# Kernel optimization log

Measured on AMD Instinct MI355X. Metric: run time of the kernel, lower is better.

Reference implementation:

```python
import jax, jax.numpy as jnp
import numpy as np

N_NODES = 100000
N_EDGES = 1600000
D_FEAT = 256
D_HID = 256


def setup_inputs() -> dict:
    key = jax.random.key(0)
    ks = jax.random.split(key, 8)
    x = jax.random.normal(ks[0], (N_NODES, D_FEAT), dtype=jnp.float32)
    src = jax.random.randint(ks[1], (N_EDGES,), 0, N_NODES, dtype=jnp.int32)
    dst = jax.random.randint(ks[2], (N_EDGES,), 0, N_NODES, dtype=jnp.int32)
    s = 1.0 / np.sqrt(D_FEAT)
    W_self1 = jax.random.normal(ks[3], (D_FEAT, D_HID), dtype=jnp.float32) * s
    W_neigh1 = jax.random.normal(ks[4], (D_FEAT, D_HID), dtype=jnp.float32) * s
    b1 = jnp.zeros((D_HID,), dtype=jnp.float32)
    s2 = 1.0 / np.sqrt(D_HID)
    W_self2 = jax.random.normal(ks[5], (D_HID, 1), dtype=jnp.float32) * s2
    W_neigh2 = jax.random.normal(ks[6], (D_HID, 1), dtype=jnp.float32) * s2
    b2 = jnp.zeros((1,), dtype=jnp.float32)
    return {"x": x, "src": src, "dst": dst,
            "W_self1": W_self1, "W_neigh1": W_neigh1, "b1": b1,
            "W_self2": W_self2, "W_neigh2": W_neigh2, "b2": b2}


def _mean_aggregate(h, src, dst, n_nodes):
    # sum of neighbor features per destination node, then divide by in-degree (clamped to 1)
    msg = jax.ops.segment_sum(h[src], dst, num_segments=n_nodes)  # [N, d]
    deg = jax.ops.segment_sum(jnp.ones((src.shape[0],), dtype=h.dtype), dst,
                              num_segments=n_nodes)
    return msg / jnp.maximum(deg, 1.0)[:, None]


def _sage_layer(h, src, dst, W_self, W_neigh, b):
    # DGL SAGEConv('mean'): h_dst @ W_self + mean_neigh(h_src) @ W_neigh + b
    neigh = _mean_aggregate(h, src, dst, h.shape[0])
    return h @ W_self + neigh @ W_neigh + b


def reference(x, src, dst, W_self1, W_neigh1, b1, W_self2, W_neigh2, b2):
    h = _sage_layer(x, src, dst, W_self1, W_neigh1, b1)
    h = jax.nn.sigmoid(h)  # F.sigmoid activation; dropout is identity in eval
    h = _sage_layer(h, src, dst, W_self2, W_neigh2, b2)  # [N, 1]
    return h
```

## Files before the change

### kernel.cpp

```cpp
#include <hip/hip_runtime.h>
#include <hip/hip_bf16.h>

typedef __attribute__((ext_vector_type(8))) short short8;
typedef __attribute__((ext_vector_type(4))) float f32x4;

__device__ __forceinline__ unsigned short f2b(float f) {
    union { float f; unsigned int u; } v; v.f = f;
    unsigned int u = v.u;
    unsigned int r = (u + 0x7fffu + ((u >> 16) & 1u)) >> 16;
    return (unsigned short)r;
}
__device__ __forceinline__ float b2f(unsigned int h) {
    union { unsigned int u; float f; } v; v.u = h << 16; return v.f;
}
__device__ __forceinline__ void acc8(uint4 v, float* a) {
    a[0] += b2f(v.x & 0xffffu); a[1] += b2f(v.x >> 16);
    a[2] += b2f(v.y & 0xffffu); a[3] += b2f(v.y >> 16);
    a[4] += b2f(v.z & 0xffffu); a[5] += b2f(v.z >> 16);
    a[6] += b2f(v.w & 0xffffu); a[7] += b2f(v.w >> 16);
}

#define DF 256
#define KK2 512
#define EPT 8
#define BCAP 8192

__global__ void k_convx(const float* __restrict__ x, unsigned short* __restrict__ xb, int total) {
    int i = (blockIdx.x * blockDim.x + threadIdx.x) * 8;
    if (i >= total) return;
    float4 v0 = *(const float4*)(x + i);
    float4 v1 = *(const float4*)(x + i + 4);
    uint4 o;
    o.x = (unsigned)f2b(v0.x) | ((unsigned)f2b(v0.y) << 16);
    o.y = (unsigned)f2b(v0.z) | ((unsigned)f2b(v0.w) << 16);
    o.z = (unsigned)f2b(v1.x) | ((unsigned)f2b(v1.y) << 16);
    o.w = (unsigned)f2b(v1.z) | ((unsigned)f2b(v1.w) << 16);
    *(uint4*)(xb + i) = o;
}

__global__ void k_buildw(const float* __restrict__ Ws1, const float* __restrict__ Wn1,
                         unsigned short* __restrict__ Wt) {
    int tid = blockIdx.x * blockDim.x + threadIdx.x;
    int n = tid >> 9, k = tid & 511;
    float v = (k < DF) ? Ws1[k * DF + n] : Wn1[(k - DF) * DF + n];
    Wt[tid] = f2b(v);
}

__global__ void k_ginit(int* __restrict__ gcur, int NB) {
    int t = blockIdx.x * blockDim.x + threadIdx.x;
    if (t < NB) gcur[t * 16] = 0;
}

__global__ __launch_bounds__(256) void k_bin(const int* __restrict__ src, const int* __restrict__ dst,
                                             int* __restrict__ gcur, unsigned* __restrict__ colidx2, int E) {
    __shared__ int cnt[512];
    int t = threadIdx.x;
    int base = blockIdx.x * (256 * EPT);
    for (int b = t; b < 512; b += 256) cnt[b] = 0;
    __syncthreads();
    unsigned pk[EPT];
#pragma unroll
    for (int i = 0; i < EPT; ++i) {
        int idx = base + t + i * 256;
        unsigned w = 0xffffffffu;
        if (idx < E) {
            int d = dst[idx];
            int b = d >> 8, dl = d & 255;
            int r = atomicAdd(&cnt[b], 1);
            w = ((unsigned)dl << 22) | ((unsigned)b << 13) | (unsigned)r;
        }
        pk[i] = w;
    }
    __syncthreads();
    for (int b = t; b < 512; b += 256) {
        int c = cnt[b];
        if (c > 0) cnt[b] = atomicAdd(&gcur[b * 16], c);
    }
    __syncthreads();
#pragma unroll
    for (int i = 0; i < EPT; ++i) {
        unsigned w = pk[i];
        if (w == 0xffffffffu) continue;
        int idx = base + t + i * 256;
        int b = (w >> 13) & 0x1FF;
        int pos = cnt[b] + (int)(w & 0x1FFF);
        if (pos < BCAP)
            colidx2[(size_t)b * BCAP + pos] = ((w >> 22) << 17) | (unsigned)src[idx];
    }
}

__global__ __launch_bounds__(512) void k_bscan(const int* __restrict__ gcur, int* __restrict__ bbase,
                                               int* __restrict__ rowptr, int NB, int N) {
    __shared__ int sm[512];
    int t = threadIdx.x;
    int c = (t < NB) ? gcur[t * 16] : 0;
    if (c > BCAP) c = BCAP;
    sm[t] = c; __syncthreads();
    for (int off = 1; off < 512; off <<= 1) {
        int u = (t >= off) ? sm[t - off] : 0;
        __syncthreads();
        sm[t] += u;
        __syncthreads();
    }
    if (t < NB) bbase[t] = sm[t] - c;
    if (t == NB - 1) rowptr[N] = sm[t];
}

__global__ __launch_bounds__(256) void k_bsort(const unsigned* __restrict__ colidx2,
                                               const int* __restrict__ gcur,
                                               const int* __restrict__ bbase,
                                               int* __restrict__ rowptr,
                                               int* __restrict__ colidx, int N) {
    __shared__ unsigned ent[BCAP];
    __shared__ unsigned short rnk[BCAP];
    __shared__ int cnt2[256], sc[256];
    int b = blockIdx.x, t = threadIdx.x;
    int lo = b << 8;
    int n = gcur[b * 16]; if (n > BCAP) n = BCAP;
    int start = bbase[b];
    const unsigned* reg = colidx2 + (size_t)b * BCAP;
    for (int i = t; i < n; i += 256) ent[i] = reg[i];
    cnt2[t] = 0;
    __syncthreads();
    for (int i = t; i < n; i += 256) {
        int d = ent[i] >> 17;
        rnk[i] = (unsigned short)atomicAdd(&cnt2[d], 1);
    }
    __syncthreads();
    int v = cnt2[t]; sc[t] = v; __syncthreads();
    for (int off = 1; off < 256; off <<= 1) {
        int u = (t >= off) ? sc[t - off] : 0;
        __syncthreads();
        sc[t] += u;
        __syncthreads();
    }
    int exc = sc[t] - v;
    if (lo + t < N) rowptr[lo + t] = start + exc;
    __syncthreads();
    sc[t] = exc;
    __syncthreads();
    for (int i = t; i < n; i += 256) {
        unsigned w = ent[i];
        int d = w >> 17;
        colidx[start + sc[d] + rnk[i]] = (int)(w & 0x1FFFFu);
    }
}

__global__ void k_agg(const unsigned short* __restrict__ xb, const int* __restrict__ rowptr,
                      const int* __restrict__ colidx, unsigned short* __restrict__ nb, int N) {
    int w = (blockIdx.x * blockDim.x + threadIdx.x) >> 6;
    int lane = threadIdx.x & 63;
    if (w >= N) return;
    int s = rowptr[w], e = rowptr[w + 1];
    int half = lane >> 5, l2 = lane & 31;
    const unsigned short* base = xb + l2 * 8;
    float a[8] = {0.f, 0.f, 0.f, 0.f, 0.f, 0.f, 0.f, 0.f};
    int j = s;
    for (; j + 15 < e; j += 16) {
        int c0 = colidx[j + half];
        int c1 = colidx[j + 2 + half];
        int c2 = colidx[j + 4 + half];
        int c3 = colidx[j + 6 + half];
        int c4 = colidx[j + 8 + half];
        int c5 = colidx[j + 10 + half];
        int c6 = colidx[j + 12 + half];
        int c7 = colidx[j + 14 + half];
        uint4 v0 = *(const uint4*)(base + (size_t)c0 * DF);
        uint4 v1 = *(const uint4*)(base + (size_t)c1 * DF);
        uint4 v2 = *(const uint4*)(base + (size_t)c2 * DF);
        uint4 v3 = *(const uint4*)(base + (size_t)c3 * DF);
        uint4 v4 = *(const uint4*)(base + (size_t)c4 * DF);
        uint4 v5 = *(const uint4*)(base + (size_t)c5 * DF);
        uint4 v6 = *(const uint4*)(base + (size_t)c6 * DF);
        uint4 v7 = *(const uint4*)(base + (size_t)c7 * DF);
        acc8(v0, a); acc8(v1, a); acc8(v2, a); acc8(v3, a);
        acc8(v4, a); acc8(v5, a); acc8(v6, a); acc8(v7, a);
    }
    for (; j + 7 < e; j += 8) {
        int c0 = colidx[j + half];
        int c1 = colidx[j + 2 + half];
        int c2 = colidx[j + 4 + half];
        int c3 = colidx[j + 6 + half];
        uint4 v0 = *(const uint4*)(base + (size_t)c0 * DF);
        uint4 v1 = *(const uint4*)(base + (size_t)c1 * DF);
        uint4 v2 = *(const uint4*)(base + (size_t)c2 * DF);
        uint4 v3 = *(const uint4*)(base + (size_t)c3 * DF);
        acc8(v0, a); acc8(v1, a); acc8(v2, a); acc8(v3, a);
    }
    for (; j + 3 < e; j += 4) {
        int c0 = colidx[j + half];
        int c1 = colidx[j + 2 + half];
        uint4 v0 = *(const uint4*)(base + (size_t)c0 * DF);
        uint4 v1 = *(const uint4*)(base + (size_t)c1 * DF);
        acc8(v0, a); acc8(v1, a);
    }
    for (; j + 1 < e; j += 2) {
        int c = colidx[j + half];
        uint4 v = *(const uint4*)(base + (size_t)c * DF);
        acc8(v, a);
    }
    if (j < e && half == 0) {
        int c = colidx[j];
        uint4 v = *(const uint4*)(base + (size_t)c * DF);
        acc8(v, a);
    }
#pragma unroll
    for (int i = 0; i < 8; ++i) a[i] += __shfl_xor(a[i], 32);
    if (half == 0) {
        float r = 1.0f / (float)((e - s) > 1 ? (e - s) : 1);
        uint4 o;
        o.x = (unsigned)f2b(a[0] * r) | ((unsigned)f2b(a[1] * r) << 16);
        o.y = (unsigned)f2b(a[2] * r) | ((unsigned)f2b(a[3] * r) << 16);
        o.z = (unsigned)f2b(a[4] * r) | ((unsigned)f2b(a[5] * r) << 16);
        o.w = (unsigned)f2b(a[6] * r) | ((unsigned)f2b(a[7] * r) << 16);
        *(uint4*)(nb + (size_t)w * DF + l2 * 8) = o;
    }
}

__global__ __launch_bounds__(512) void k_gemm(const unsigned short* __restrict__ xb,
                                              const unsigned short* __restrict__ nbm,
                                              const unsigned short* __restrict__ Wt,
                                              const float* __restrict__ b1,
                                              const float* __restrict__ Ws2,
                                              const float* __restrict__ Wn2,
                                              float* __restrict__ sv,
                                              float* __restrict__ tv, int M) {
    __shared__ __align__(16) unsigned short As[128 * 64];
    __shared__ __align__(16) unsigned short Bs[256 * 64];
    const int tid = threadIdx.x, lane = tid & 63, wave = tid >> 6;
    const int wr = wave >> 2, wc = wave & 3;
    const int bm = blockIdx.x;
    f32x4 acc[4][4] = {};
    for (int kt = 0; kt < 8; ++kt) {
        int k0 = kt * 64;
#pragma unroll
        for (int q = 0; q < 2; ++q) {
            int unit = q * 512 + tid;
            int row = unit >> 3, kc = (unit & 7) * 8;
            int grow = bm * 128 + row; if (grow >= M) grow = M - 1;
            int k = k0 + kc;
            const unsigned short* srcA = (k < DF) ? xb + (size_t)grow * DF + k
                                                  : nbm + (size_t)grow * DF + (k - DF);
            __builtin_amdgcn_global_load_lds(
                (const __attribute__((address_space(1))) void*)srcA,
                (__attribute__((address_space(3))) void*)&As[unit * 8],
                16, 0, 0);
        }
#pragma unroll
        for (int q = 0; q < 4; ++q) {
            int unit = q * 512 + tid;
            int row = unit >> 3, kc = (unit & 7) * 8;
            const unsigned short* srcB = Wt + (size_t)row * KK2 + k0 + kc;
            __builtin_amdgcn_global_load_lds(
                (const __attribute__((address_space(1))) void*)srcB,
                (__attribute__((address_space(3))) void*)&Bs[unit * 8],
                16, 0, 0);
        }
        __syncthreads();
#pragma unroll
        for (int kk = 0; kk < 2; ++kk) {
            short8 af[4], bf[4];
            int kl = kk * 32 + (lane >> 4) * 8;
#pragma unroll
            for (int m = 0; m < 4; ++m)
                af[m] = *(const short8*)&As[(wr * 64 + m * 16 + (lane & 15)) * 64 + kl];
#pragma unroll
            for (int n = 0; n < 4; ++n)
                bf[n] = *(const short8*)&Bs[(wc * 64 + n * 16 + (lane & 15)) * 64 + kl];
#pragma unroll
            for (int m = 0; m < 4; ++m)
#pragma unroll
                for (int n = 0; n < 4; ++n)
                    acc[m][n] = __builtin_amdgcn_mfma_f32_16x16x32_bf16(af[m], bf[n], acc[m][n], 0, 0, 0);
        }
        __syncthreads();
    }
    float bias[4], w2s[4], w2n[4];
#pragma unroll
    for (int n = 0; n < 4; ++n) {
        int col = wc * 64 + n * 16 + (lane & 15);
        bias[n] = b1[col];
        w2s[n] = Ws2[col];
        w2n[n] = Wn2[col];
    }
    float* sred = (float*)As;
#pragma unroll
    for (int m = 0; m < 4; ++m)
#pragma unroll
        for (int r = 0; r < 4; ++r) {
            int row128 = wr * 64 + m * 16 + (lane >> 4) * 4 + r;
            float ps = 0.f, pt = 0.f;
#pragma unroll
            for (int n = 0; n < 4; ++n) {
                float v = acc[m][n][r] + bias[n];
                float sg = 1.f / (1.f + expf(-v));
                ps += sg * w2s[n];
                pt += sg * w2n[n];
            }
#pragma unroll
            for (int o = 1; o < 16; o <<= 1) {
                ps += __shfl_xor(ps, o);
                pt += __shfl_xor(pt, o);
            }
            if ((lane & 15) == 0) {
                sred[row128 * 4 + wc] = ps;
                sred[2048 + row128 * 4 + wc] = pt;
            }
        }
    __syncthreads();
    if (tid < 128) {
        int grow = bm * 128 + tid;
        if (grow < M) {
            sv[grow] = sred[tid * 4] + sred[tid * 4 + 1] + sred[tid * 4 + 2] + sred[tid * 4 + 3];
            tv[grow] = sred[2048 + tid * 4] + sred[2048 + tid * 4 + 1] +
                       sred[2048 + tid * 4 + 2] + sred[2048 + tid * 4 + 3];
        }
    }
}

__global__ void k_out(const float* __restrict__ sv, const float* __restrict__ tv,
                      const int* __restrict__ rowptr, const int* __restrict__ colidx,
                      const float* __restrict__ b2, float* __restrict__ out, int N) {
    int i = blockIdx.x * blockDim.x + threadIdx.x;
    if (i >= N) return;
    int a = rowptr[i], b = rowptr[i + 1];
    float sum = 0.f;
    for (int j = a; j < b; ++j) sum += tv[colidx[j]];
    out[i] = sv[i] + sum / (float)((b - a) > 1 ? (b - a) : 1) + b2[0];
}

extern "C" void kernel_launch(void* const* d_in, const int* in_sizes, int n_in,
                              void* d_out, int out_size, void* d_ws, size_t ws_size,
                              hipStream_t stream) {
    const float* x   = (const float*)d_in[0];
    const int*   src = (const int*)d_in[1];
    const int*   dst = (const int*)d_in[2];
    const float* Ws1 = (const float*)d_in[3];
    const float* Wn1 = (const float*)d_in[4];
    const float* b1  = (const float*)d_in[5];
    const float* Ws2 = (const float*)d_in[6];
    const float* Wn2 = (const float*)d_in[7];
    const float* b2  = (const float*)d_in[8];
    float* out = (float*)d_out;

    const int N = in_sizes[0] / DF;
    const int E = in_sizes[1];
    const int NB = (N + 255) >> 8;

    char* w = (char*)d_ws;
    auto carve = [&](size_t bytes) { char* p = w; w += ((bytes + 255) / 256) * 256; return p; };
    float* sv   = (float*)carve((size_t)N * 4);
    float* tv   = (float*)carve((size_t)N * 4);
    unsigned short* xb  = (unsigned short*)carve((size_t)N * DF * 2);
    unsigned short* nbm = (unsigned short*)carve((size_t)N * DF * 2);
    unsigned short* Wt  = (unsigned short*)carve((size_t)KK2 * DF * 2);
    int* rowptr = (int*)carve((size_t)(N + 1) * 4);
    int* colidx = (int*)carve((size_t)E * 4);
    unsigned* colidx2 = (unsigned*)carve((size_t)NB * BCAP * 4);
    int* gcur   = (int*)carve((size_t)NB * 16 * 4);
    int* bbase  = (int*)carve(512 * 4);

    int totalx = N * DF;
    k_convx<<<dim3((totalx / 8 + 255) / 256), dim3(256), 0, stream>>>(x, xb, totalx);
    k_buildw<<<dim3((KK2 * DF) / 256), dim3(256), 0, stream>>>(Ws1, Wn1, Wt);
    k_ginit<<<dim3((NB + 255) / 256), dim3(256), 0, stream>>>(gcur, NB);

    k_bin<<<dim3((E + 256 * EPT - 1) / (256 * EPT)), dim3(256), 0, stream>>>(src, dst, gcur, colidx2, E);
    k_bscan<<<dim3(1), dim3(512), 0, stream>>>(gcur, bbase, rowptr, NB, N);
    k_bsort<<<dim3(NB), dim3(256), 0, stream>>>(colidx2, gcur, bbase, rowptr, colidx, N);

    k_agg<<<dim3((N + 3) / 4), dim3(256), 0, stream>>>(xb, rowptr, colidx, nbm, N);

    k_gemm<<<dim3((N + 127) / 128), dim3(512), 0, stream>>>(xb, nbm, Wt, b1, Ws2, Wn2, sv, tv, N);

    k_out<<<dim3((N + 255) / 256), dim3(256), 0, stream>>>(sv, tv, rowptr, colidx, b2, out, N);
}
```

Before: 427.0 us.

## Gather neighbor features as FP8 copy and merge prep kernels into one launch

The prep kernel now also writes an FP8 (e4m3) copy of x alongside the bf16 copy. The aggregation kernel gathers 8-byte FP8 rows instead of 16-byte bf16 rows and converts them with hardware pack-convert instructions, halving the bytes moved by the gather. The three setup kernels (x conversion, weight transpose, counter init) are combined into one launch, and the 16-wide unroll in aggregation is dropped. FP8 quantization of neighbor features lowers accuracy of the mean aggregation and could break tolerance, and writing the extra xq array adds some store traffic.

After: 380.1 us. -11.0%, faster.

```diff
diff --git a/kernel.cpp b/kernel.cpp
--- a/kernel.cpp
+++ b/kernel.cpp
@@ -3,6 +3,7 @@
 
 typedef __attribute__((ext_vector_type(8))) short short8;
 typedef __attribute__((ext_vector_type(4))) float f32x4;
+typedef __attribute__((ext_vector_type(2))) float f32x2;
 
 __device__ __forceinline__ unsigned short f2b(float f) {
     union { float f; unsigned int u; } v; v.f = f;
@@ -13,11 +14,13 @@
 __device__ __forceinline__ float b2f(unsigned int h) {
     union { unsigned int u; float f; } v; v.u = h << 16; return v.f;
 }
-__device__ __forceinline__ void acc8(uint4 v, float* a) {
-    a[0] += b2f(v.x & 0xffffu); a[1] += b2f(v.x >> 16);
-    a[2] += b2f(v.y & 0xffffu); a[3] += b2f(v.y >> 16);
-    a[4] += b2f(v.z & 0xffffu); a[5] += b2f(v.z >> 16);
-    a[6] += b2f(v.w & 0xffffu); a[7] += b2f(v.w >> 16);
+__device__ __forceinline__ void accq(uint2 v, float* a) {
+    f32x2 f0 = __builtin_amdgcn_cvt_pk_f32_fp8((int)v.x, false);
+    f32x2 f1 = __builtin_amdgcn_cvt_pk_f32_fp8((int)v.x, true);
+    f32x2 f2 = __builtin_amdgcn_cvt_pk_f32_fp8((int)v.y, false);
+    f32x2 f3 = __builtin_amdgcn_cvt_pk_f32_fp8((int)v.y, true);
+    a[0] += f0.x; a[1] += f0.y; a[2] += f1.x; a[3] += f1.y;
+    a[4] += f2.x; a[5] += f2.y; a[6] += f3.x; a[7] += f3.y;
 }
 
 #define DF 256
@@ -25,30 +28,41 @@
 #define EPT 8
 #define BCAP 8192
 
-__global__ void k_convx(const float* __restrict__ x, unsigned short* __restrict__ xb, int total) {
-    int i = (blockIdx.x * blockDim.x + threadIdx.x) * 8;
-    if (i >= total) return;
-    float4 v0 = *(const float4*)(x + i);
-    float4 v1 = *(const float4*)(x + i + 4);
-    uint4 o;
-    o.x = (unsigned)f2b(v0.x) | ((unsigned)f2b(v0.y) << 16);
-    o.y = (unsigned)f2b(v0.z) | ((unsigned)f2b(v0.w) << 16);
-    o.z = (unsigned)f2b(v1.x) | ((unsigned)f2b(v1.y) << 16);
-    o.w = (unsigned)f2b(v1.z) | ((unsigned)f2b(v1.w) << 16);
-    *(uint4*)(xb + i) = o;
-}
-
-__global__ void k_buildw(const float* __restrict__ Ws1, const float* __restrict__ Wn1,
-                         unsigned short* __restrict__ Wt) {
-    int tid = blockIdx.x * blockDim.x + threadIdx.x;
-    int n = tid >> 9, k = tid & 511;
-    float v = (k < DF) ? Ws1[k * DF + n] : Wn1[(k - DF) * DF + n];
-    Wt[tid] = f2b(v);
-}
-
-__global__ void k_ginit(int* __restrict__ gcur, int NB) {
-    int t = blockIdx.x * blockDim.x + threadIdx.x;
-    if (t < NB) gcur[t * 16] = 0;
+__global__ __launch_bounds__(256) void k_prep(const float* __restrict__ x,
+                                              const float* __restrict__ Ws1,
+                                              const float* __restrict__ Wn1,
+                                              unsigned short* __restrict__ xb,
+                                              unsigned char* __restrict__ xq,
+                                              unsigned short* __restrict__ Wt,
+                                              int* __restrict__ gcur,
+                                              int CB, int totalx, int NB) {
+    int bid = blockIdx.x, tid = threadIdx.x;
+    if (bid < CB) {
+        int i = (bid * 256 + tid) * 8;
+        if (i >= totalx) return;
+        float4 v0 = *(const float4*)(x + i);
+        float4 v1 = *(const float4*)(x + i + 4);
+        uint4 o;
+        o.x = (unsigned)f2b(v0.x) | ((unsigned)f2b(v0.y) << 16);
+        o.y = (unsigned)f2b(v0.z) | ((unsigned)f2b(v0.w) << 16);
+        o.z = (unsigned)f2b(v1.x) | ((unsigned)f2b(v1.y) << 16);
+        o.w = (unsigned)f2b(v1.z) | ((unsigned)f2b(v1.w) << 16);
+        *(uint4*)(xb + i) = o;
+        unsigned q0 = (unsigned)__builtin_amdgcn_cvt_pk_fp8_f32(v0.x, v0.y, 0, false);
+        q0 = (unsigned)__builtin_amdgcn_cvt_pk_fp8_f32(v0.z, v0.w, (int)q0, true);
+        unsigned q1 = (unsigned)__builtin_amdgcn_cvt_pk_fp8_f32(v1.x, v1.y, 0, false);
+        q1 = (unsigned)__builtin_amdgcn_cvt_pk_fp8_f32(v1.z, v1.w, (int)q1, true);
+        uint2 q; q.x = q0; q.y = q1;
+        *(uint2*)(xq + i) = q;
+    } else if (bid < CB + 512) {
+        int t2 = (bid - CB) * 256 + tid;
+        int n = t2 >> 9, k = t2 & 511;
+        float v = (k < DF) ? Ws1[k * DF + n] : Wn1[(k - DF) * DF + n];
+        Wt[t2] = f2b(v);
+    } else {
+        int t2 = (bid - CB - 512) * 256 + tid;
+        if (t2 < NB) gcur[t2 * 16] = 0;
+    }
 }
 
 __global__ __launch_bounds__(256) void k_bin(const int* __restrict__ src, const int* __restrict__ dst,
@@ -146,63 +160,43 @@
     }
 }
 
-__global__ void k_agg(const unsigned short* __restrict__ xb, const int* __restrict__ rowptr,
-                      const int* __restrict__ colidx, unsigned short* __restrict__ nb, int N) {
+__global__ void k_agg(const unsigned char* __restrict__ xq, const int* __restrict__ rowptr,
+                      const int* __restrict__ colidx, unsigned short* __restrict__ nbm, int N) {
     int w = (blockIdx.x * blockDim.x + threadIdx.x) >> 6;
     int lane = threadIdx.x & 63;
     if (w >= N) return;
     int s = rowptr[w], e = rowptr[w + 1];
     int half = lane >> 5, l2 = lane & 31;
-    const unsigned short* base = xb + l2 * 8;
+    const unsigned char* base = xq + l2 * 8;
     float a[8] = {0.f, 0.f, 0.f, 0.f, 0.f, 0.f, 0.f, 0.f};
     int j = s;
-    for (; j + 15 < e; j += 16) {
-        int c0 = colidx[j + half];
-        int c1 = colidx[j + 2 + half];
-        int c2 = colidx[j + 4 + half];
-        int c3 = colidx[j + 6 + half];
-        int c4 = colidx[j + 8 + half];
-        int c5 = colidx[j + 10 + half];
-        int c6 = colidx[j + 12 + half];
-        int c7 = colidx[j + 14 + half];
-        uint4 v0 = *(const uint4*)(base + (size_t)c0 * DF);
-        uint4 v1 = *(const uint4*)(base + (size_t)c1 * DF);
-        uint4 v2 = *(const uint4*)(base + (size_t)c2 * DF);
-        uint4 v3 = *(const uint4*)(base + (size_t)c3 * DF);
-        uint4 v4 = *(const uint4*)(base + (size_t)c4 * DF);
-        uint4 v5 = *(const uint4*)(base + (size_t)c5 * DF);
-        uint4 v6 = *(const uint4*)(base + (size_t)c6 * DF);
-        uint4 v7 = *(const uint4*)(base + (size_t)c7 * DF);
-        acc8(v0, a); acc8(v1, a); acc8(v2, a); acc8(v3, a);
-        acc8(v4, a); acc8(v5, a); acc8(v6, a); acc8(v7, a);
-    }
     for (; j + 7 < e; j += 8) {
         int c0 = colidx[j + half];
         int c1 = colidx[j + 2 + half];
         int c2 = colidx[j + 4 + half];
         int c3 = colidx[j + 6 + half];
-        uint4 v0 = *(const uint4*)(base + (size_t)c0 * DF);
-        uint4 v1 = *(const uint4*)(base + (size_t)c1 * DF);
-        uint4 v2 = *(const uint4*)(base + (size_t)c2 * DF);
-        uint4 v3 = *(const uint4*)(base + (size_t)c3 * DF);
-        acc8(v0, a); acc8(v1, a); acc8(v2, a); acc8(v3, a);
+        uint2 v0 = *(const uint2*)(base + (size_t)c0 * DF);
+        uint2 v1 = *(const uint2*)(base + (size_t)c1 * DF);
+        uint2 v2 = *(const uint2*)(base + (size_t)c2 * DF);
+        uint2 v3 = *(const uint2*)(base + (size_t)c3 * DF);
+        accq(v0, a); accq(v1, a); accq(v2, a); accq(v3, a);
     }
     for (; j + 3 < e; j += 4) {
         int c0 = colidx[j + half];
         int c1 = colidx[j + 2 + half];
-        uint4 v0 = *(const uint4*)(base + (size_t)c0 * DF);
-        uint4 v1 = *(const uint4*)(base + (size_t)c1 * DF);
-        acc8(v0, a); acc8(v1, a);
+        uint2 v0 = *(const uint2*)(base + (size_t)c0 * DF);
+        uint2 v1 = *(const uint2*)(base + (size_t)c1 * DF);
+        accq(v0, a); accq(v1, a);
     }
     for (; j + 1 < e; j += 2) {
         int c = colidx[j + half];
-        uint4 v = *(const uint4*)(base + (size_t)c * DF);
-        acc8(v, a);
+        uint2 v = *(const uint2*)(base + (size_t)c * DF);
+        accq(v, a);
     }
     if (j < e && half == 0) {
         int c = colidx[j];
-        uint4 v = *(const uint4*)(base + (size_t)c * DF);
-        acc8(v, a);
+        uint2 v = *(const uint2*)(base + (size_t)c * DF);
+        accq(v, a);
     }
 #pragma unroll
     for (int i = 0; i < 8; ++i) a[i] += __shfl_xor(a[i], 32);
@@ -213,7 +207,7 @@
         o.y = (unsigned)f2b(a[2] * r) | ((unsigned)f2b(a[3] * r) << 16);
         o.z = (unsigned)f2b(a[4] * r) | ((unsigned)f2b(a[5] * r) << 16);
         o.w = (unsigned)f2b(a[6] * r) | ((unsigned)f2b(a[7] * r) << 16);
-        *(uint4*)(nb + (size_t)w * DF + l2 * 8) = o;
+        *(uint4*)(nbm + (size_t)w * DF + l2 * 8) = o;
     }
 }
 
@@ -346,12 +340,14 @@
     const int N = in_sizes[0] / DF;
     const int E = in_sizes[1];
     const int NB = (N + 255) >> 8;
+    const int totalx = N * DF;
 
     char* w = (char*)d_ws;
     auto carve = [&](size_t bytes) { char* p = w; w += ((bytes + 255) / 256) * 256; return p; };
     float* sv   = (float*)carve((size_t)N * 4);
     float* tv   = (float*)carve((size_t)N * 4);
     unsigned short* xb  = (unsigned short*)carve((size_t)N * DF * 2);
+    unsigned char*  xq  = (unsigned char*)carve((size_t)N * DF);
     unsigned short* nbm = (unsigned short*)carve((size_t)N * DF * 2);
     unsigned short* Wt  = (unsigned short*)carve((size_t)KK2 * DF * 2);
     int* rowptr = (int*)carve((size_t)(N + 1) * 4);
@@ -360,16 +356,16 @@
     int* gcur   = (int*)carve((size_t)NB * 16 * 4);
     int* bbase  = (int*)carve(512 * 4);
 
-    int totalx = N * DF;
-    k_convx<<<dim3((totalx / 8 + 255) / 256), dim3(256), 0, stream>>>(x, xb, totalx);
-    k_buildw<<<dim3((KK2 * DF) / 256), dim3(256), 0, stream>>>(Ws1, Wn1, Wt);
-    k_ginit<<<dim3((NB + 255) / 256), dim3(256), 0, stream>>>(gcur, NB);
+    const int CB = (totalx / 8 + 255) / 256;
+    const int GB = (NB + 255) / 256;
+    k_prep<<<dim3(CB + 512 + GB), dim3(256), 0, stream>>>(x, Ws1, Wn1, xb, xq, Wt, gcur,
+                                                          CB, totalx, NB);
 
     k_bin<<<dim3((E + 256 * EPT - 1) / (256 * EPT)), dim3(256), 0, stream>>>(src, dst, gcur, colidx2, E);
     k_bscan<<<dim3(1), dim3(512), 0, stream>>>(gcur, bbase, rowptr, NB, N);
     k_bsort<<<dim3(NB), dim3(256), 0, stream>>>(colidx2, gcur, bbase, rowptr, colidx, N);
 
-    k_agg<<<dim3((N + 3) / 4), dim3(256), 0, stream>>>(xb, rowptr, colidx, nbm, N);
+    k_agg<<<dim3((N + 3) / 4), dim3(256), 0, stream>>>(xq, rowptr, colidx, nbm, N);
 
     k_gemm<<<dim3((N + 127) / 128), dim3(512), 0, stream>>>(xb, nbm, Wt, b1, Ws2, Wn2, sv, tv, N);
 
```
